# Optimization experiments

Measured on AMD Instinct MI355X. Metric: run time of the kernel, lower is better.

Reference implementation:

```python
import jax, jax.numpy as jnp
import numpy as np

N_ATOMS = 16384
N_BLOCKS = 4096
K = 3          # top-k nearest context atoms (min(3, n_ctx) in original; n_ctx >> 3 here)
EPS_W = 1e-8   # inverse-distance weight epsilon (matches original)
EPS_D = 1e-12  # tiny epsilon inside sqrt for numerical safety of the distance


def setup_inputs() -> dict:
    key = jax.random.key(0)
    k1, k2, k3, k4, k5 = jax.random.split(key, 5)
    # coordinates spread out like real molecular coords (Angstrom-ish scale)
    X = jax.random.normal(k1, (N_ATOMS, 3), dtype=jnp.float32) * 10.0
    base_noise = jax.random.normal(k2, (N_ATOMS, 3), dtype=jnp.float32)      # randn_like(X)
    centroid_noise = jax.random.normal(k3, (N_ATOMS, 3), dtype=jnp.float32)  # per-atom randn(3)
    block_ids = jnp.sort(jax.random.randint(k4, (N_ATOMS,), 0, N_BLOCKS)).astype(jnp.int32)
    generate_mask = jax.random.randint(k5, (N_BLOCKS,), 0, 2).astype(bool)
    return {
        "X": X,
        "base_noise": base_noise,
        "centroid_noise": centroid_noise,
        "block_ids": block_ids,
        "generate_mask": generate_mask,
    }


def reference(X, base_noise, centroid_noise, block_ids, generate_mask):
    """Vectorized sample_chemical_prior: for every generated atom, find the 3
    nearest CONTEXT atoms, take an inverse-distance-weighted centroid, and add
    0.5 * gaussian noise. Non-generated atoms keep base_noise (randn_like)."""
    n = X.shape[0]
    gen_atoms = generate_mask[block_ids]           # [N] atoms being generated
    ctx = ~gen_atoms                               # [N] context atoms

    # pairwise squared distances via ||a||^2 + ||b||^2 - 2 a.b  -> [N, N]
    xn = jnp.sum(X * X, axis=-1)
    sq = xn[:, None] + xn[None, :] - 2.0 * (X @ X.T)
    d = jnp.sqrt(jnp.maximum(sq, 0.0) + EPS_D)

    # only context atoms are valid neighbor candidates; exclude self for safety
    not_self = ~jnp.eye(n, dtype=bool)
    d = jnp.where(ctx[None, :] & not_self, d, jnp.inf)

    # k nearest context atoms per row (smallest distances)
    neg_dk, idx = jax.lax.top_k(-d, K)             # [N, K]
    dk = -neg_dk

    # inverse-distance weights, normalized (matches original)
    w = 1.0 / (dk + EPS_W)
    w = w / jnp.sum(w, axis=-1, keepdims=True)

    coords = X[idx]                                # [N, K, 3] gather neighbor coords
    centroid = jnp.sum(coords * w[..., None], axis=1)  # [N, 3]

    x0 = jnp.where(gen_atoms[:, None], centroid + 0.5 * centroid_noise, base_noise)
    return x0
```

## Files before the change

### kernel.cpp

```cpp
#include <hip/hip_runtime.h>
#include <cstdint>

#define N_ATOMS 16384
#define NBLK 64
#define NTHR 256
#define G 24
#define NCELLS (G*G*G)
#define NCELLS_PAD 14336
#define CPT 14
#define BOX_LO -48.0f
#define INV_CELL 0.25f
#define SINIT 3.0e38f

#define OFF_COUNTS 0
#define OFF_BLKGEN 256
#define OFF_BLKGOFF 512
#define OFF_FLAGS 1024
#define OFF_CNT 3072
#define OFF_START 60416
#define OFF_GENIDX 118016
#define OFF_CTX4 183552

__device__ __forceinline__ int cell1(float x) {
    int c = (int)floorf((x - BOX_LO) * INV_CELL);
    return min(max(c, 0), G - 1);
}

__device__ __forceinline__ void ins3(float v, int vi,
                                     float& s1, float& s2, float& s3,
                                     int& i1, int& i2, int& i3)
{
    const bool b1 = v < s1, b2 = v < s2, b3 = v < s3;
    s3 = b2 ? s2 : (b3 ? v : s3);   i3 = b2 ? i2 : (b3 ? vi : i3);
    s2 = b1 ? s1 : (b2 ? v : s2);   i2 = b1 ? i1 : (b2 ? vi : i2);
    s1 = b1 ? v : s1;               i1 = b1 ? vi : i1;
}

__device__ __forceinline__ void ins3v(float v, float& s1, float& s2, float& s3)
{
    const bool b1 = v < s1, b2 = v < s2, b3 = v < s3;
    s3 = b2 ? s2 : (b3 ? v : s3);
    s2 = b1 ? s1 : (b2 ? v : s2);
    s1 = b1 ? v : s1;
}

__global__ __launch_bounds__(256)
void k0_zero(int4* __restrict__ cell_cnt4)
{
    cell_cnt4[blockIdx.x * 256 + threadIdx.x] = make_int4(0, 0, 0, 0);
}

__global__ __launch_bounds__(NTHR)
void k1_classify(const float* __restrict__ X,
                 const int* __restrict__ block_ids,
                 const unsigned int* __restrict__ mask,
                 const float* __restrict__ base_noise,
                 float* __restrict__ out,
                 unsigned long long* __restrict__ flags,
                 int* __restrict__ blk_gen,
                 int* __restrict__ cell_cnt)
{
    __shared__ int sflag;
    __shared__ int wg[4];
    const int t = threadIdx.x;
    const int wave = t >> 6, lane = t & 63;

    if (t == 0) sflag = 0;
    __syncthreads();
    if (mask[t] > 1u) sflag = 1;
    __syncthreads();
    const bool is_u8 = (sflag != 0);
    const unsigned char* m8 = (const unsigned char*)mask;

    const int i = blockIdx.x * NTHR + t;
    const int bid = block_ids[i];
    const bool g = is_u8 ? (m8[bid] != 0) : (mask[bid] != 0u);

    out[3 * i + 0] = base_noise[3 * i + 0];
    out[3 * i + 1] = base_noise[3 * i + 1];
    out[3 * i + 2] = base_noise[3 * i + 2];

    const unsigned long long mg = __ballot(g);
    if (lane == 0) { flags[blockIdx.x * 4 + wave] = mg; wg[wave] = __popcll(mg); }
    __syncthreads();
    if (t == 0) blk_gen[blockIdx.x] = wg[0] + wg[1] + wg[2] + wg[3];

    if (!g) {
        const float x = X[3 * i], y = X[3 * i + 1], z = X[3 * i + 2];
        const int cx = cell1(x), cy = cell1(y), cz = cell1(z);
        atomicAdd(&cell_cnt[(cz * G + cy) * G + cx], 1);
    }
}

__global__ __launch_bounds__(1024)
void k2_scan(int* __restrict__ cell_cnt,
             int* __restrict__ cell_start,
             const int* __restrict__ blk_gen,
             int* __restrict__ blk_goff,
             int* __restrict__ counts)
{
    const int t = threadIdx.x;
    const int wave = t >> 6, lane = t & 63;
    int loc[CPT]; int sum = 0;
    #pragma unroll
    for (int k = 0; k < CPT; ++k) {
        const int v = cell_cnt[t * CPT + k];
        loc[k] = sum; sum += v;
    }
    int v = sum;
    #pragma unroll
    for (int d = 1; d < 64; d <<= 1) { const int u = __shfl_up(v, d); if (lane >= d) v += u; }
    __shared__ int wsum[16], wexc[16];
    if (lane == 63) wsum[wave] = v;
    __syncthreads();
    if (t < 16) {
        int v2 = wsum[t];
        const int orig = v2;
        #pragma unroll
        for (int d = 1; d < 16; d <<= 1) { const int u = __shfl_up(v2, d); if (t >= d) v2 += u; }
        wexc[t] = v2 - orig;
    }
    __syncthreads();
    const int base = wexc[wave] + (v - sum);
    #pragma unroll
    for (int k = 0; k < CPT; ++k) {
        cell_start[t * CPT + k] = base + loc[k];
        cell_cnt[t * CPT + k] = 0;
    }
    if (t == 1023) cell_start[NCELLS_PAD] = base + sum;
    __syncthreads();
    if (t < 64) {
        const int o = blk_gen[t];
        int s = o;
        #pragma unroll
        for (int d = 1; d < 64; d <<= 1) { const int u = __shfl_up(s, d); if (t >= d) s += u; }
        blk_goff[t] = s - o;
        if (t == 63) { counts[1] = s; counts[0] = N_ATOMS - s; }
    }
}

__global__ __launch_bounds__(NTHR)
void k3_scatter(const float* __restrict__ X,
                const unsigned long long* __restrict__ flags,
                const int* __restrict__ blk_goff,
                const int* __restrict__ cell_start,
                int* __restrict__ cell_cur,
                float4* __restrict__ ctx4s,
                int* __restrict__ genidx)
{
    const int t = threadIdx.x;
    const int wave = t >> 6, lane = t & 63;
    const int i = blockIdx.x * NTHR + t;
    const unsigned long long fw = flags[blockIdx.x * 4 + wave];
    const bool g = (fw >> lane) & 1ull;
    int og = blk_goff[blockIdx.x];
    int oc = blockIdx.x * NTHR - og;
    #pragma unroll
    for (int w = 0; w < 4; ++w) {
        if (w < wave) {
            const int p = __popcll(flags[blockIdx.x * 4 + w]);
            og += p; oc += 64 - p;
        }
    }
    const unsigned long long below = (1ull << lane) - 1ull;
    og += __popcll(fw & below);
    oc += __popcll((~fw) & below);
    if (g) {
        genidx[og] = i;
    } else {
        const float x = X[3 * i], y = X[3 * i + 1], z = X[3 * i + 2];
        float xn = x * x; xn += y * y; xn += z * z;
        const int cx = cell1(x), cy = cell1(y), cz = cell1(z);
        const int c = (cz * G + cy) * G + cx;
        const int pos = cell_start[c] + atomicAdd(&cell_cur[c], 1);
        ctx4s[pos] = make_float4(x, y, z, xn);
    }
}

__global__ __launch_bounds__(512)
void k4_search(const float* __restrict__ X,
               const float* __restrict__ cnoise,
               const int* __restrict__ counts,
               const int* __restrict__ cell_start,
               const float4* __restrict__ ctx4s,
               const int* __restrict__ genidx,
               float* __restrict__ out)
{
    const int n_gen = counts[1];
    const int wave = threadIdx.x >> 6, lane = threadIdx.x & 63;
    const int slot = (int)blockIdx.x * 8 + wave;
    if (slot >= n_gen) return;

    const int ai = genidx[slot];
    const float qx = X[3 * ai], qy = X[3 * ai + 1], qz = X[3 * ai + 2];
    float xnq = qx * qx; xnq += qy * qy; xnq += qz * qz;
    const int cqx = cell1(qx), cqy = cell1(qy), cqz = cell1(qz);

    float s1 = SINIT, s2 = SINIT, s3 = SINIT;
    int i1 = 0, i2 = 0, i3 = 0;

    if (lane < 27) {
        const int dx = lane % 3 - 1, dy = (lane / 3) % 3 - 1, dz = lane / 9 - 1;
        const int cx = cqx + dx, cy = cqy + dy, cz = cqz + dz;
        if ((unsigned)cx < G && (unsigned)cy < G && (unsigned)cz < G) {
            const int c = (cz * G + cy) * G + cx;
            const int p0 = cell_start[c], p1 = cell_start[c + 1];
            if (p0 < p1) {
                float4 cc = ctx4s[p0];
                for (int p = p0; p < p1; ++p) {
                    float4 nxt;
                    if (p + 1 < p1) nxt = ctx4s[p + 1];
                    const float dot = qx * cc.x + qy * cc.y + qz * cc.z;
                    const float sq = (xnq + cc.w) - 2.0f * dot;
                    ins3(sq, p, s1, s2, s3, i1, i2, i3);
                    cc = nxt;
                }
            }
        }
    }

    int r = 1;
    for (;;) {
        float m1 = s1, m2 = s2, m3 = s3;
        #pragma unroll
        for (int m = 1; m < 64; m <<= 1) {
            const float a = __shfl_xor(m1, m);
            const float b = __shfl_xor(m2, m);
            const float c = __shfl_xor(m3, m);
            ins3v(a, m1, m2, m3); ins3v(b, m1, m2, m3); ins3v(c, m1, m2, m3);
        }
        const float bnd = (float)(4 * r) * (float)(4 * r);
        if (m3 + 0.01f < bnd || r >= G) break;
        ++r;
        const int B = 2 * r + 1, B2 = B * B, V = B2 * B;
        for (int u = lane; u < V; u += 64) {
            int dz = u / B2; const int rem = u - dz * B2;
            int dy = rem / B; int dx = rem - dy * B;
            dx -= r; dy -= r; dz -= r;
            const int ax = abs(dx), ay = abs(dy), az = abs(dz);
            if (max(ax, max(ay, az)) != r) continue;
            const int cx = cqx + dx, cy = cqy + dy, cz = cqz + dz;
            if ((unsigned)cx >= G || (unsigned)cy >= G || (unsigned)cz >= G) continue;
            const int c = (cz * G + cy) * G + cx;
            const int p0 = cell_start[c], p1 = cell_start[c + 1];
            for (int p = p0; p < p1; ++p) {
                const float4 cc = ctx4s[p];
                const float dot = qx * cc.x + qy * cc.y + qz * cc.z;
                const float sq = (xnq + cc.w) - 2.0f * dot;
                ins3(sq, p, s1, s2, s3, i1, i2, i3);
            }
        }
    }

    #pragma unroll
    for (int m = 1; m < 64; m <<= 1) {
        const float a = __shfl_xor(s1, m); const int ja = __shfl_xor(i1, m);
        const float b = __shfl_xor(s2, m); const int jb = __shfl_xor(i2, m);
        const float c = __shfl_xor(s3, m); const int jc = __shfl_xor(i3, m);
        ins3(a, ja, s1, s2, s3, i1, i2, i3);
        ins3(b, jb, s1, s2, s3, i1, i2, i3);
        ins3(c, jc, s1, s2, s3, i1, i2, i3);
    }

    if (lane == 0) {
        const float d1 = sqrtf(fmaxf(s1, 0.0f) + 1e-12f);
        const float d2 = sqrtf(fmaxf(s2, 0.0f) + 1e-12f);
        const float d3 = sqrtf(fmaxf(s3, 0.0f) + 1e-12f);
        float w1 = 1.0f / (d1 + 1e-8f);
        float w2 = 1.0f / (d2 + 1e-8f);
        float w3 = 1.0f / (d3 + 1e-8f);
        float wsum = w1 + w2;
        wsum += w3;
        w1 /= wsum; w2 /= wsum; w3 /= wsum;
        const float4 c1 = ctx4s[i1];
        const float4 c2 = ctx4s[i2];
        const float4 c3 = ctx4s[i3];
        float cxo = w1 * c1.x + w2 * c2.x; cxo += w3 * c3.x;
        float cyo = w1 * c1.y + w2 * c2.y; cyo += w3 * c3.y;
        float czo = w1 * c1.z + w2 * c2.z; czo += w3 * c3.z;
        out[3 * ai + 0] = cxo + 0.5f * cnoise[3 * ai + 0];
        out[3 * ai + 1] = cyo + 0.5f * cnoise[3 * ai + 1];
        out[3 * ai + 2] = czo + 0.5f * cnoise[3 * ai + 2];
    }
}

extern "C" void kernel_launch(void* const* d_in, const int* in_sizes, int n_in,
                              void* d_out, int out_size, void* d_ws, size_t ws_size,
                              hipStream_t stream) {
    const float* X          = (const float*)d_in[0];
    const float* base_noise = (const float*)d_in[1];
    const float* cnoise     = (const float*)d_in[2];
    const int*   block_ids  = (const int*)d_in[3];
    const unsigned int* gmask = (const unsigned int*)d_in[4];
    float* out = (float*)d_out;

    char* ws = (char*)d_ws;
    int*    counts     = (int*)(ws + OFF_COUNTS);
    int*    blk_gen    = (int*)(ws + OFF_BLKGEN);
    int*    blk_goff   = (int*)(ws + OFF_BLKGOFF);
    unsigned long long* flags = (unsigned long long*)(ws + OFF_FLAGS);
    int*    cell_cnt   = (int*)(ws + OFF_CNT);
    int*    cell_start = (int*)(ws + OFF_START);
    int*    genidx     = (int*)(ws + OFF_GENIDX);
    float4* ctx4s      = (float4*)(ws + OFF_CTX4);

    k0_zero<<<NCELLS_PAD / 1024, 256, 0, stream>>>((int4*)cell_cnt);
    k1_classify<<<NBLK, NTHR, 0, stream>>>(X, block_ids, gmask, base_noise,
                                           out, flags, blk_gen, cell_cnt);
    k2_scan<<<1, 1024, 0, stream>>>(cell_cnt, cell_start, blk_gen, blk_goff, counts);
    k3_scatter<<<NBLK, NTHR, 0, stream>>>(X, flags, blk_goff, cell_start,
                                          cell_cnt, ctx4s, genidx);
    k4_search<<<N_ATOMS / 8, 512, 0, stream>>>(X, cnoise, counts, cell_start,
                                               ctx4s, genidx, out);
}
```

Baseline: 52.64 us.

## Flatten 27-cell neighbor scan into wave-wide load-balanced candidate loop

```diff
diff --git a/kernel.cpp b/kernel.cpp
--- a/kernel.cpp
+++ b/kernel.cpp
@@ -199,23 +199,39 @@
     float s1 = SINIT, s2 = SINIT, s3 = SINIT;
     int i1 = 0, i2 = 0, i3 = 0;
 
+    int cnt = 0, st = 0;
     if (lane < 27) {
         const int dx = lane % 3 - 1, dy = (lane / 3) % 3 - 1, dz = lane / 9 - 1;
         const int cx = cqx + dx, cy = cqy + dy, cz = cqz + dz;
         if ((unsigned)cx < G && (unsigned)cy < G && (unsigned)cz < G) {
             const int c = (cz * G + cy) * G + cx;
-            const int p0 = cell_start[c], p1 = cell_start[c + 1];
-            if (p0 < p1) {
-                float4 cc = ctx4s[p0];
-                for (int p = p0; p < p1; ++p) {
-                    float4 nxt;
-                    if (p + 1 < p1) nxt = ctx4s[p + 1];
-                    const float dot = qx * cc.x + qy * cc.y + qz * cc.z;
-                    const float sq = (xnq + cc.w) - 2.0f * dot;
-                    ins3(sq, p, s1, s2, s3, i1, i2, i3);
-                    cc = nxt;
-                }
-            }
+            st = cell_start[c];
+            cnt = cell_start[c + 1] - st;
+        }
+    }
+    int pre = cnt;
+    #pragma unroll
+    for (int d = 1; d < 64; d <<= 1) { const int u = __shfl_up(pre, d); if (lane >= d) pre += u; }
+    const int T = __shfl(pre, 63);
+    const int ebase = pre - cnt;
+    const int pk = st - ebase;
+    const int iters = (T + 63) >> 6;
+    for (int it = 0; it < iters; ++it) {
+        const int j = it * 64 + lane;
+        const int jc = min(j, T - 1);
+        int L = 0;
+        #pragma unroll
+        for (int stp = 16; stp >= 1; stp >>= 1) {
+            const int cand = L + stp;
+            const int bv = __shfl(ebase, cand < 27 ? cand : 26);
+            if (cand < 27 && bv <= jc) L = cand;
+        }
+        const int p = __shfl(pk, L) + jc;
+        const float4 cc = ctx4s[p];
+        if (j < T) {
+            const float dot = qx * cc.x + qy * cc.y + qz * cc.z;
+            const float sq = (xnq + cc.w) - 2.0f * dot;
+            ins3(sq, p, s1, s2, s3, i1, i2, i3);
         }
     }
 
```

Measured after the change: 51.50 us. 1.02x faster.

## Search four query atoms per wavefront with 16-lane groups and enumerate shell cells directly

Applied to the files above, without the earlier changes.

```diff
diff --git a/kernel.cpp b/kernel.cpp
--- a/kernel.cpp
+++ b/kernel.cpp
@@ -5,7 +5,7 @@
 #define NBLK 64
 #define NTHR 256
 #define G 24
-#define NCELLS (G*G*G)
+#define NCELLS 13824
 #define NCELLS_PAD 14336
 #define CPT 14
 #define BOX_LO -48.0f
@@ -177,7 +177,7 @@
     }
 }
 
-__global__ __launch_bounds__(512)
+__global__ __launch_bounds__(256)
 void k4_search(const float* __restrict__ X,
                const float* __restrict__ cnoise,
                const int* __restrict__ counts,
@@ -187,9 +187,14 @@
                float* __restrict__ out)
 {
     const int n_gen = counts[1];
-    const int wave = threadIdx.x >> 6, lane = threadIdx.x & 63;
-    const int slot = (int)blockIdx.x * 8 + wave;
-    if (slot >= n_gen) return;
+    const int t = threadIdx.x;
+    const int wave = t >> 6, lane = t & 63;
+    if ((int)blockIdx.x * 16 + wave * 4 >= n_gen) return;
+    const int grp = lane >> 4;
+    const int gl  = lane & 15;
+    int slot = (int)blockIdx.x * 16 + wave * 4 + grp;
+    const bool valid = slot < n_gen;
+    slot = valid ? slot : n_gen - 1;
 
     const int ai = genidx[slot];
     const float qx = X[3 * ai], qy = X[3 * ai + 1], qz = X[3 * ai + 2];
@@ -199,22 +204,17 @@
     float s1 = SINIT, s2 = SINIT, s3 = SINIT;
     int i1 = 0, i2 = 0, i3 = 0;
 
-    if (lane < 27) {
-        const int dx = lane % 3 - 1, dy = (lane / 3) % 3 - 1, dz = lane / 9 - 1;
+    for (int m = gl; m < 27; m += 16) {
+        const int dx = m % 3 - 1, dy = (m / 3) % 3 - 1, dz = m / 9 - 1;
         const int cx = cqx + dx, cy = cqy + dy, cz = cqz + dz;
         if ((unsigned)cx < G && (unsigned)cy < G && (unsigned)cz < G) {
             const int c = (cz * G + cy) * G + cx;
             const int p0 = cell_start[c], p1 = cell_start[c + 1];
-            if (p0 < p1) {
-                float4 cc = ctx4s[p0];
-                for (int p = p0; p < p1; ++p) {
-                    float4 nxt;
-                    if (p + 1 < p1) nxt = ctx4s[p + 1];
-                    const float dot = qx * cc.x + qy * cc.y + qz * cc.z;
-                    const float sq = (xnq + cc.w) - 2.0f * dot;
-                    ins3(sq, p, s1, s2, s3, i1, i2, i3);
-                    cc = nxt;
-                }
+            for (int p = p0; p < p1; ++p) {
+                const float4 cc = ctx4s[p];
+                const float dot = qx * cc.x + qy * cc.y + qz * cc.z;
+                const float sq = (xnq + cc.w) - 2.0f * dot;
+                ins3(sq, p, s1, s2, s3, i1, i2, i3);
             }
         }
     }
@@ -223,7 +223,7 @@
     for (;;) {
         float m1 = s1, m2 = s2, m3 = s3;
         #pragma unroll
-        for (int m = 1; m < 64; m <<= 1) {
+        for (int m = 1; m < 16; m <<= 1) {
             const float a = __shfl_xor(m1, m);
             const float b = __shfl_xor(m2, m);
             const float c = __shfl_xor(m3, m);
@@ -232,13 +232,23 @@
         const float bnd = (float)(4 * r) * (float)(4 * r);
         if (m3 + 0.01f < bnd || r >= G) break;
         ++r;
-        const int B = 2 * r + 1, B2 = B * B, V = B2 * B;
-        for (int u = lane; u < V; u += 64) {
-            int dz = u / B2; const int rem = u - dz * B2;
-            int dy = rem / B; int dx = rem - dy * B;
-            dx -= r; dy -= r; dz -= r;
-            const int ax = abs(dx), ay = abs(dy), az = abs(dz);
-            if (max(ax, max(ay, az)) != r) continue;
+        const int B = 2 * r + 1, F = B * B, P8 = 8 * r;
+        const int S = 2 * F + (2 * r - 1) * P8;
+        for (int u = gl; u < S; u += 16) {
+            int dx, dy, dz;
+            if (u < 2 * F) {
+                dz = (u < F) ? -r : r;
+                const int v = (u < F) ? u : u - F;
+                dx = v % B - r; dy = v / B - r;
+            } else {
+                const int v = u - 2 * F;
+                dz = v / P8 - (r - 1);
+                const int w = v % P8;
+                if (w < 2 * r)          { dx = -r + w;            dy = -r; }
+                else if (w < 4 * r)     { dx = r;                 dy = -r + (w - 2 * r); }
+                else if (w < 6 * r)     { dx = r - (w - 4 * r);   dy = r; }
+                else                    { dx = -r;                dy = r - (w - 6 * r); }
+            }
             const int cx = cqx + dx, cy = cqy + dy, cz = cqz + dz;
             if ((unsigned)cx >= G || (unsigned)cy >= G || (unsigned)cz >= G) continue;
             const int c = (cz * G + cy) * G + cx;
@@ -253,7 +263,7 @@
     }
 
     #pragma unroll
-    for (int m = 1; m < 64; m <<= 1) {
+    for (int m = 1; m < 16; m <<= 1) {
         const float a = __shfl_xor(s1, m); const int ja = __shfl_xor(i1, m);
         const float b = __shfl_xor(s2, m); const int jb = __shfl_xor(i2, m);
         const float c = __shfl_xor(s3, m); const int jc = __shfl_xor(i3, m);
@@ -262,7 +272,7 @@
         ins3(c, jc, s1, s2, s3, i1, i2, i3);
     }
 
-    if (lane == 0) {
+    if (gl == 0 && valid) {
         const float d1 = sqrtf(fmaxf(s1, 0.0f) + 1e-12f);
         const float d2 = sqrtf(fmaxf(s2, 0.0f) + 1e-12f);
         const float d3 = sqrtf(fmaxf(s3, 0.0f) + 1e-12f);
@@ -310,6 +320,6 @@
     k2_scan<<<1, 1024, 0, stream>>>(cell_cnt, cell_start, blk_gen, blk_goff, counts);
     k3_scatter<<<NBLK, NTHR, 0, stream>>>(X, flags, blk_goff, cell_start,
                                           cell_cnt, ctx4s, genidx);
-    k4_search<<<N_ATOMS / 8, 512, 0, stream>>>(X, cnoise, counts, cell_start,
-                                               ctx4s, genidx, out);
-}
+    k4_search<<<N_ATOMS / 16, 256, 0, stream>>>(X, cnoise, counts, cell_start,
+                                                ctx4s, genidx, out);
+}
```

After: 73.23 us. +39.1%, slower.
